# Kernel optimization log

Measured on AMD Instinct MI355X. Metric: run time of the kernel, lower is better.

The kernel has to match this reference:

```python
import jax, jax.numpy as jnp
import numpy as np

L, D, F, H, E, V = 16, 256, 512, 8, 12, 52000  # layers, width, FFWidth, heads, experts, vocab
B, S = 4, 512
HD = D // H
EPS = 1e-5


def _ln(x, s, b):
    m = x.mean(-1, keepdims=True)
    v = ((x - m) ** 2).mean(-1, keepdims=True)
    return (x - m) / jnp.sqrt(v + EPS) * s + b


def setup_inputs() -> dict:
    key = jax.random.key(0)
    ks = jax.random.split(key, 12)
    w = lambda k, shape: (jax.random.normal(k, shape, dtype=jnp.float32) * 0.02)
    return {
        "tokens": jax.random.randint(ks[0], (B, S), 0, V),
        "emb": w(ks[1], (V, D)),
        "Wq": w(ks[2], (L, D, D)), "bq": jnp.zeros((L, D), jnp.float32),
        "Wk": w(ks[3], (L, D, D)), "bk": jnp.zeros((L, D), jnp.float32),
        "Wv": w(ks[4], (L, D, D)), "bv": jnp.zeros((L, D), jnp.float32),
        "ln1_s": jnp.ones((L, D), jnp.float32), "ln1_b": jnp.zeros((L, D), jnp.float32),
        "ln2_s": jnp.ones((L, D), jnp.float32), "ln2_b": jnp.zeros((L, D), jnp.float32),
        "gW": w(ks[5], (L, D, E)), "gb": jnp.zeros((L, E), jnp.float32),
        "ff1W": w(ks[6], (L, E, D, F)), "ff1b": jnp.zeros((L, E, F), jnp.float32),
        "ffGW": w(ks[7], (L, E, D, F)), "ffGb": jnp.zeros((L, E, F), jnp.float32),
        "ff2W": w(ks[8], (L, E, F, D)), "ff2b": jnp.zeros((L, E, D), jnp.float32),
    }


def _forward(tokens, emb, Wq, bq, Wk, bk, Wv, bv, ln1_s, ln1_b, ln2_s, ln2_b,
             gW, gb, ff1W, ff1b, ffGW, ffGb, ff2W, ff2b):
    x = emb[tokens]  # [B,S,D]
    causal = jnp.triu(jnp.full((S, S), -jnp.inf, dtype=x.dtype), 1)

    def body(x, p):
        (wq, bq_, wk, bk_, wv, bv_, l1s, l1b, l2s, l2b,
         gw, gb_, f1w, f1b, fgw, fgb, f2w, f2b) = p
        q = (x @ wq + bq_).reshape(B, S, H, HD)
        k = (x @ wk + bk_).reshape(B, S, H, HD)
        v = (x @ wv + bv_).reshape(B, S, H, HD)
        # NOTE: original applies no 1/sqrt(d) scaling -- kept faithful
        att = jnp.einsum('bshw,bShw->bhsS', q, k) + causal
        att = jax.nn.softmax(att, axis=-1)
        o = jnp.einsum('bhsS,bShw->bshw', att, v).reshape(B, S, D)
        norm = _ln(o + x, l1s, l1b)
        # MoE: top-2 experts, outputs SUMMED (no gate weighting, per original)
        probs = jax.nn.softmax(norm @ gw + gb_, axis=-1)
        _, idx = jax.lax.top_k(probs, 2)  # [B,S,2]
        msk = jax.nn.one_hot(idx, E, dtype=norm.dtype).sum(-2)  # [B,S,E] in {0,1}
        h = jax.nn.silu(jnp.einsum('bsd,edf->bsef', norm, f1w) + f1b) \
            * (jnp.einsum('bsd,edf->bsef', norm, fgw) + fgb)
        y = jnp.einsum('bsef,efd->bsed', h, f2w) + f2b
        moe = jnp.einsum('bsed,bse->bsd', y, msk)
        return _ln(moe + norm, l2s, l2b), None

    x, _ = jax.lax.scan(body, x, (Wq, bq, Wk, bk, Wv, bv, ln1_s, ln1_b, ln2_s, ln2_b,
                                  gW, gb, ff1W, ff1b, ffGW, ffGb, ff2W, ff2b))
    return x


def reference(tokens, emb, Wq, bq, Wk, bk, Wv, bv, ln1_s, ln1_b, ln2_s, ln2_b,
              gW, gb, ff1W, ff1b, ffGW, ffGb, ff2W, ff2b):
    return _forward(tokens, emb, Wq, bq, Wk, bk, Wv, bv, ln1_s, ln1_b, ln2_s, ln2_b,
                    gW, gb, ff1W, ff1b, ffGW, ffGb, ff2W, ff2b)
```

## Files before the change

kernel.cpp:

```cpp
#include <hip/hip_runtime.h>
#include <math.h>

#define LNUM 16
#define D 256
#define FF 512
#define NH 8
#define NE 12
#define HD 32
#define BB 4
#define SS 512
#define NT 2048
#define EPS 1e-5f
#define CAP 512
#define ROWSP (NE * CAP)

typedef _Float16 f16;
typedef __attribute__((ext_vector_type(8))) _Float16 f16x8;
typedef __attribute__((ext_vector_type(4))) _Float16 f16x4;
typedef __attribute__((ext_vector_type(4))) float f32x4;
#define MFMA(A, B, C) __builtin_amdgcn_mfma_f32_16x16x32_f16((A), (B), (C), 0, 0, 0)

__device__ inline void splitf(float x, f16& h, f16& l) {
  f16 hh = (f16)x;
  h = hh;
  l = (f16)(x - (float)hh);
}

__global__ __launch_bounds__(256) void k_wprep(const float* __restrict__ src,
                                               f16* __restrict__ dh, f16* __restrict__ dl,
                                               int K, int N) {
  const size_t msz = (size_t)K * N * blockIdx.z;
  src += msz; dh += msz; dl += msz;
  const int n0 = blockIdx.x * 32, k0 = blockIdx.y * 32;
  __shared__ f16 th[32][36], tl[32][36];
  const int t = threadIdx.x;
  {
    const int r = t >> 3, c4 = (t & 7) * 4;
    float4 v = *(const float4*)(src + (size_t)(k0 + r) * N + n0 + c4);
    f16 h0, l0, h1, l1, h2, l2, h3, l3;
    splitf(v.x, h0, l0); splitf(v.y, h1, l1);
    splitf(v.z, h2, l2); splitf(v.w, h3, l3);
    th[c4 + 0][r] = h0; tl[c4 + 0][r] = l0;
    th[c4 + 1][r] = h1; tl[c4 + 1][r] = l1;
    th[c4 + 2][r] = h2; tl[c4 + 2][r] = l2;
    th[c4 + 3][r] = h3; tl[c4 + 3][r] = l3;
  }
  __syncthreads();
  const int rn = t >> 3, ck = (t & 7) * 4;
  f16x4 hv, lv;
#pragma unroll
  for (int j = 0; j < 4; j++) { hv[j] = th[rn][ck + j]; lv[j] = tl[rn][ck + j]; }
  *(f16x4*)(dh + (size_t)(n0 + rn) * K + k0 + ck) = hv;
  *(f16x4*)(dl + (size_t)(n0 + rn) * K + k0 + ck) = lv;
}

__global__ __launch_bounds__(256) void k_embed(const int* __restrict__ tok,
                                               const float* __restrict__ emb,
                                               float* __restrict__ x,
                                               f16* __restrict__ xh, f16* __restrict__ xl,
                                               int* __restrict__ cntbuf) {
  int n = blockIdx.x, t = threadIdx.x;
  if (n == 0 && t < LNUM * NE) cntbuf[t] = 0;
  float val = emb[(size_t)tok[n] * D + t];
  x[(size_t)n * D + t] = val;
  f16 h, l; splitf(val, h, l);
  xh[(size_t)n * D + t] = h;
  xl[(size_t)n * D + t] = l;
}

__global__ __launch_bounds__(256) void k_qkv_mfma(
    const f16* __restrict__ xh, const f16* __restrict__ xl,
    const f16* __restrict__ wqh, const f16* __restrict__ wql, const float* __restrict__ bq,
    const f16* __restrict__ wkh, const f16* __restrict__ wkl, const float* __restrict__ bk,
    const f16* __restrict__ wvh, const f16* __restrict__ wvl, const float* __restrict__ bv,
    f16* __restrict__ qhb, f16* __restrict__ qlb,
    f16* __restrict__ khb, f16* __restrict__ klb,
    f16* __restrict__ vhb, f16* __restrict__ vlb) {
  const int mat = blockIdx.z;
  const f16* Wh; const f16* Wl; const float* bias; f16* outh; f16* outl;
  if (mat == 0)      { Wh = wqh; Wl = wql; bias = bq; outh = qhb; outl = qlb; }
  else if (mat == 1) { Wh = wkh; Wl = wkl; bias = bk; outh = khb; outl = klb; }
  else               { Wh = wvh; Wl = wvl; bias = bv; outh = vhb; outl = vlb; }
  const int row0 = blockIdx.x * 128, col0 = blockIdx.y * 64;
  __shared__ f16 Ah[128][44], Al[128][44], Bh[64][44], Bl[64][44];
  const int tid = threadIdx.x;
  const int asr = tid >> 1, asc = (tid & 1) * 16;
  const int bn2 = tid >> 2, bkc = (tid & 3) * 8;
  const int lane = tid & 63, w = tid >> 6;
  const int lm = lane & 15, lg = lane >> 4, lk = lg * 8;
  f32x4 acc[2][4] = {};
  for (int k0 = 0; k0 < D; k0 += 32) {
    {
      size_t ga = (size_t)(row0 + asr) * D + k0 + asc;
      *(f16x8*)&Ah[asr][asc]     = *(const f16x8*)(xh + ga);
      *(f16x8*)&Ah[asr][asc + 8] = *(const f16x8*)(xh + ga + 8);
      *(f16x8*)&Al[asr][asc]     = *(const f16x8*)(xl + ga);
      *(f16x8*)&Al[asr][asc + 8] = *(const f16x8*)(xl + ga + 8);
      size_t gb = (size_t)(col0 + bn2) * D + k0 + bkc;
      *(f16x8*)&Bh[bn2][bkc] = *(const f16x8*)(Wh + gb);
      *(f16x8*)&Bl[bn2][bkc] = *(const f16x8*)(Wl + gb);
    }
    __syncthreads();
    f16x8 a_h[2], a_l[2];
#pragma unroll
    for (int mt = 0; mt < 2; mt++) {
      a_h[mt] = *(const f16x8*)&Ah[w * 32 + mt * 16 + lm][lk];
      a_l[mt] = *(const f16x8*)&Al[w * 32 + mt * 16 + lm][lk];
    }
#pragma unroll
    for (int nt = 0; nt < 4; nt++) {
      f16x8 b_h = *(const f16x8*)&Bh[nt * 16 + lm][lk];
      f16x8 b_l = *(const f16x8*)&Bl[nt * 16 + lm][lk];
#pragma unroll
      for (int mt = 0; mt < 2; mt++) {
        f32x4 c = acc[mt][nt];
        c = MFMA(a_h[mt], b_h, c);
        c = MFMA(a_h[mt], b_l, c);
        c = MFMA(a_l[mt], b_h, c);
        acc[mt][nt] = c;
      }
    }
    __syncthreads();
  }
#pragma unroll
  for (int mt = 0; mt < 2; mt++)
#pragma unroll
    for (int nt = 0; nt < 4; nt++) {
      int col = col0 + nt * 16 + lm;
      float bv_ = bias[col];
#pragma unroll
      for (int r = 0; r < 4; r++) {
        int row = row0 + w * 32 + mt * 16 + lg * 4 + r;
        float val = acc[mt][nt][r] + bv_;
        f16 h16, l16; splitf(val, h16, l16);
        outh[(size_t)row * D + col] = h16;
        outl[(size_t)row * D + col] = l16;
      }
    }
}

__global__ __launch_bounds__(256) void k_attn_mfma(
    const f16* __restrict__ qh, const f16* __restrict__ ql,
    const f16* __restrict__ kh, const f16* __restrict__ kl,
    const f16* __restrict__ vh, const f16* __restrict__ vl,
    float* __restrict__ o) {
  const int rt = blockIdx.x, bh = blockIdx.y;
  const int b = bh >> 3, h = bh & 7;
  const int row0 = rt * 64;
  __shared__ f16 Qh[64][40], Ql[64][40], Kh[64][40], Kl[64][40];
  __shared__ f16 Vth[32][72], Vtl[32][72];
  __shared__ f16 Ph[4][16][72], Pl[4][16][72];
  const int tid = threadIdx.x;
  const int lane = tid & 63, w = tid >> 6;
  const int lm = lane & 15, lg = lane >> 4, lk = lg * 8;
  const int sr = tid >> 2, sc = (tid & 3) * 8;
  {
    size_t gq = (size_t)(b * SS + row0 + sr) * D + h * HD + sc;
    *(f16x8*)&Qh[sr][sc] = *(const f16x8*)(qh + gq);
    *(f16x8*)&Ql[sr][sc] = *(const f16x8*)(ql + gq);
  }
  f32x4 accO[2] = {};
  float mrow[4], lsum[4];
#pragma unroll
  for (int r = 0; r < 4; r++) { mrow[r] = -1e30f; lsum[r] = 0.f; }
  for (int ct = 0; ct <= rt; ct++) {
    __syncthreads();
    {
      size_t gk = (size_t)(b * SS + ct * 64 + sr) * D + h * HD + sc;
      *(f16x8*)&Kh[sr][sc] = *(const f16x8*)(kh + gk);
      *(f16x8*)&Kl[sr][sc] = *(const f16x8*)(kl + gk);
      f16x8 hv = *(const f16x8*)(vh + gk);
      f16x8 lv = *(const f16x8*)(vl + gk);
#pragma unroll
      for (int j = 0; j < 8; j++) { Vth[sc + j][sr] = hv[j]; Vtl[sc + j][sr] = lv[j]; }
    }
    __syncthreads();
    f16x8 qfh = *(const f16x8*)&Qh[w * 16 + lm][lk];
    f16x8 qfl = *(const f16x8*)&Ql[w * 16 + lm][lk];
    f32x4 s[4];
    __builtin_amdgcn_s_setprio(1);
#pragma unroll
    for (int nt = 0; nt < 4; nt++) {
      f16x8 kfh = *(const f16x8*)&Kh[nt * 16 + lm][lk];
      f16x8 kfl = *(const f16x8*)&Kl[nt * 16 + lm][lk];
      f32x4 c = {};
      c = MFMA(qfh, kfh, c);
      c = MFMA(qfh, kfl, c);
      c = MFMA(qfl, kfh, c);
      s[nt] = c;
    }
    __builtin_amdgcn_s_setprio(0);
    if (ct == rt) {
#pragma unroll
      for (int nt = 0; nt < 4; nt++)
#pragma unroll
        for (int r = 0; r < 4; r++)
          if (nt * 16 + lm > w * 16 + lg * 4 + r) s[nt][r] = -1e30f;
    }
    float scal[4];
#pragma unroll
    for (int r = 0; r < 4; r++) {
      float mt2 = fmaxf(fmaxf(s[0][r], s[1][r]), fmaxf(s[2][r], s[3][r]));
      mt2 = fmaxf(mt2, __shfl_xor(mt2, 1));
      mt2 = fmaxf(mt2, __shfl_xor(mt2, 2));
      mt2 = fmaxf(mt2, __shfl_xor(mt2, 4));
      mt2 = fmaxf(mt2, __shfl_xor(mt2, 8));
      float mn = fmaxf(mrow[r], mt2);
      scal[r] = expf(mrow[r] - mn);
      mrow[r] = mn;
    }
    float rs[4] = {0.f, 0.f, 0.f, 0.f};
#pragma unroll
    for (int nt = 0; nt < 4; nt++)
#pragma unroll
      for (int r = 0; r < 4; r++) {
        float pv = expf(s[nt][r] - mrow[r]);
        rs[r] += pv;
        f16 ph16, pl16; splitf(pv, ph16, pl16);
        Ph[w][lg * 4 + r][nt * 16 + lm] = ph16;
        Pl[w][lg * 4 + r][nt * 16 + lm] = pl16;
      }
#pragma unroll
    for (int r = 0; r < 4; r++) {
      rs[r] += __shfl_xor(rs[r], 1);
      rs[r] += __shfl_xor(rs[r], 2);
      rs[r] += __shfl_xor(rs[r], 4);
      rs[r] += __shfl_xor(rs[r], 8);
      lsum[r] = lsum[r] * scal[r] + rs[r];
      accO[0][r] *= scal[r];
      accO[1][r] *= scal[r];
    }
    __builtin_amdgcn_s_setprio(1);
#pragma unroll
    for (int ct2 = 0; ct2 < 2; ct2++)
#pragma unroll
      for (int ks = 0; ks < 2; ks++) {
        f16x8 pa_h = *(const f16x8*)&Ph[w][lm][ks * 32 + lk];
        f16x8 pa_l = *(const f16x8*)&Pl[w][lm][ks * 32 + lk];
        f16x8 vb_h = *(const f16x8*)&Vth[ct2 * 16 + lm][ks * 32 + lk];
        f16x8 vb_l = *(const f16x8*)&Vtl[ct2 * 16 + lm][ks * 32 + lk];
        accO[ct2] = MFMA(pa_h, vb_h, accO[ct2]);
        accO[ct2] = MFMA(pa_h, vb_l, accO[ct2]);
        accO[ct2] = MFMA(pa_l, vb_h, accO[ct2]);
      }
    __builtin_amdgcn_s_setprio(0);
  }
#pragma unroll
  for (int ct2 = 0; ct2 < 2; ct2++)
#pragma unroll
    for (int r = 0; r < 4; r++) {
      int grow = row0 + w * 16 + lg * 4 + r;
      o[(size_t)(b * SS + grow) * D + h * HD + ct2 * 16 + lm] = accO[ct2][r] / lsum[r];
    }
}

__global__ __launch_bounds__(256) void k_ln1gate(
    const float* __restrict__ o, const float* __restrict__ x,
    const float* __restrict__ s1, const float* __restrict__ b1,
    const float* __restrict__ gW, const float* __restrict__ gb,
    float* __restrict__ norm, f16* __restrict__ nhb, f16* __restrict__ nlb,
    int* __restrict__ cnt, int* __restrict__ rlist, int* __restrict__ tokpos) {
  const int w = threadIdx.x >> 6, lane = threadIdx.x & 63;
  const int n = blockIdx.x * 4 + w;
  float val[4], s1v = 0.f, s2v = 0.f;
#pragma unroll
  for (int j = 0; j < 4; j++) {
    int d = lane + 64 * j;
    float v = o[(size_t)n * D + d] + x[(size_t)n * D + d];
    val[j] = v; s1v += v; s2v += v * v;
  }
#pragma unroll
  for (int m = 1; m < 64; m <<= 1) {
    s1v += __shfl_xor(s1v, m);
    s2v += __shfl_xor(s2v, m);
  }
  float mean = s1v * (1.f / D);
  float var = s2v * (1.f / D) - mean * mean;
  float rstd = rsqrtf(var + EPS);
  float ge[NE];
#pragma unroll
  for (int e = 0; e < NE; e++) ge[e] = 0.f;
#pragma unroll
  for (int j = 0; j < 4; j++) {
    int d = lane + 64 * j;
    float nv = (val[j] - mean) * rstd * s1[d] + b1[d];
    norm[(size_t)n * D + d] = nv;
    f16 h16, l16; splitf(nv, h16, l16);
    nhb[(size_t)n * D + d] = h16;
    nlb[(size_t)n * D + d] = l16;
    const float* gr = gW + (size_t)d * NE;
#pragma unroll
    for (int e = 0; e < NE; e++) ge[e] += nv * gr[e];
  }
#pragma unroll
  for (int m = 1; m < 64; m <<= 1)
#pragma unroll
    for (int e = 0; e < NE; e++) ge[e] += __shfl_xor(ge[e], m);
  if (lane == 0) {
#pragma unroll
    for (int e = 0; e < NE; e++) ge[e] += gb[e];
    int i1 = 0; float v1 = ge[0];
#pragma unroll
    for (int e = 1; e < NE; e++) if (ge[e] > v1) { v1 = ge[e]; i1 = e; }
    int i2 = -1; float v2 = -3.4e38f;
#pragma unroll
    for (int e = 0; e < NE; e++) if (e != i1 && ge[e] > v2) { v2 = ge[e]; i2 = e; }
    int p1 = atomicAdd(&cnt[i1], 1);
    int row1 = i1 * CAP + p1;
    rlist[row1] = n;
    tokpos[n * 2 + 0] = row1;
    int p2 = atomicAdd(&cnt[i2], 1);
    int row2 = i2 * CAP + p2;
    rlist[row2] = n;
    tokpos[n * 2 + 1] = row2;
  }
}

__global__ __launch_bounds__(256) void k_ff1_mfma(
    const f16* __restrict__ nhb, const f16* __restrict__ nlb,
    const int* __restrict__ cnt, const int* __restrict__ rlist,
    const f16* __restrict__ w1th, const f16* __restrict__ w1tl, const float* __restrict__ b1f,
    const f16* __restrict__ wgth, const f16* __restrict__ wgtl, const float* __restrict__ bgf,
    f16* __restrict__ hhb, f16* __restrict__ hlb) {
  const int e = blockIdx.x >> 2, tl = blockIdx.x & 3;
  const int cnt_e = cnt[e];
  if (tl * 128 >= cnt_e) return;
  const int nv0 = cnt_e - tl * 128;
  const int nv = nv0 < 128 ? nv0 : 128;
  const int base = e * CAP + tl * 128;
  const int col0 = blockIdx.y * 64;
  const f16* W1h = w1th + (size_t)e * D * FF + (size_t)col0 * D;
  const f16* W1l = w1tl + (size_t)e * D * FF + (size_t)col0 * D;
  const f16* Wgh = wgth + (size_t)e * D * FF + (size_t)col0 * D;
  const f16* Wgl = wgtl + (size_t)e * D * FF + (size_t)col0 * D;
  __shared__ f16 Ah[128][44], Al[128][44];
  __shared__ f16 B1h[64][44], B1l[64][44], B2h[64][44], B2l[64][44];
  __shared__ int rows[128];
  const int tid = threadIdx.x;
  if (tid < 128) rows[tid] = (tid < nv) ? rlist[base + tid] : 0;
  __syncthreads();
  const int asr = tid >> 1, asc = (tid & 1) * 16;
  const int bn2 = tid >> 2, bkc = (tid & 3) * 8;
  const int lane = tid & 63, w = tid >> 6;
  const int lm = lane & 15, lg = lane >> 4, lk = lg * 8;
  f32x4 acc1[2][4] = {}, acc2[2][4] = {};
  const int arow = rows[asr];
  for (int k0 = 0; k0 < D; k0 += 32) {
    {
      size_t ga = (size_t)arow * D + k0 + asc;
      *(f16x8*)&Ah[asr][asc]     = *(const f16x8*)(nhb + ga);
      *(f16x8*)&Ah[asr][asc + 8] = *(const f16x8*)(nhb + ga + 8);
      *(f16x8*)&Al[asr][asc]     = *(const f16x8*)(nlb + ga);
      *(f16x8*)&Al[asr][asc + 8] = *(const f16x8*)(nlb + ga + 8);
      size_t gb = (size_t)bn2 * D + k0 + bkc;
      *(f16x8*)&B1h[bn2][bkc] = *(const f16x8*)(W1h + gb);
      *(f16x8*)&B1l[bn2][bkc] = *(const f16x8*)(W1l + gb);
      *(f16x8*)&B2h[bn2][bkc] = *(const f16x8*)(Wgh + gb);
      *(f16x8*)&B2l[bn2][bkc] = *(const f16x8*)(Wgl + gb);
    }
    __syncthreads();
    f16x8 a_h[2], a_l[2];
#pragma unroll
    for (int mt = 0; mt < 2; mt++) {
      a_h[mt] = *(const f16x8*)&Ah[w * 32 + mt * 16 + lm][lk];
      a_l[mt] = *(const f16x8*)&Al[w * 32 + mt * 16 + lm][lk];
    }
#pragma unroll
    for (int nt = 0; nt < 4; nt++) {
      f16x8 b_h = *(const f16x8*)&B1h[nt * 16 + lm][lk];
      f16x8 b_l = *(const f16x8*)&B1l[nt * 16 + lm][lk];
      f16x8 c_h = *(const f16x8*)&B2h[nt * 16 + lm][lk];
      f16x8 c_l = *(const f16x8*)&B2l[nt * 16 + lm][lk];
#pragma unroll
      for (int mt = 0; mt < 2; mt++) {
        f32x4 c1 = acc1[mt][nt];
        c1 = MFMA(a_h[mt], b_h, c1);
        c1 = MFMA(a_h[mt], b_l, c1);
        c1 = MFMA(a_l[mt], b_h, c1);
        acc1[mt][nt] = c1;
        f32x4 c2 = acc2[mt][nt];
        c2 = MFMA(a_h[mt], c_h, c2);
        c2 = MFMA(a_h[mt], c_l, c2);
        c2 = MFMA(a_l[mt], c_h, c2);
        acc2[mt][nt] = c2;
      }
    }
    __syncthreads();
  }
#pragma unroll
  for (int mt = 0; mt < 2; mt++)
#pragma unroll
    for (int nt = 0; nt < 4; nt++) {
      int col = col0 + nt * 16 + lm;
      float bb1 = b1f[e * FF + col], bb2 = bgf[e * FF + col];
#pragma unroll
      for (int r = 0; r < 4; r++) {
        int rit = w * 32 + mt * 16 + lg * 4 + r;
        if (rit < nv) {
          float z1 = acc1[mt][nt][r] + bb1;
          float zg = acc2[mt][nt][r] + bb2;
          float sl = z1 / (1.f + expf(-z1));
          float hv = sl * zg;
          f16 h16, l16; splitf(hv, h16, l16);
          hhb[(size_t)(base + rit) * FF + col] = h16;
          hlb[(size_t)(base + rit) * FF + col] = l16;
        }
      }
    }
}

__global__ __launch_bounds__(256) void k_ff2_mfma(
    const f16* __restrict__ hhb, const f16* __restrict__ hlb,
    const int* __restrict__ cnt,
    const f16* __restrict__ w2th, const f16* __restrict__ w2tl, const float* __restrict__ b2f,
    float* __restrict__ ybuf) {
  const int e = blockIdx.x >> 2, tl = blockIdx.x & 3;
  const int cnt_e = cnt[e];
  if (tl * 128 >= cnt_e) return;
  const int nv0 = cnt_e - tl * 128;
  const int nv = nv0 < 128 ? nv0 : 128;
  const int base = e * CAP + tl * 128;
  const int col0 = blockIdx.y * 64;
  const f16* W2h = w2th + (size_t)e * FF * D + (size_t)col0 * FF;
  const f16* W2l = w2tl + (size_t)e * FF * D + (size_t)col0 * FF;
  __shared__ f16 Ah[128][44], Al[128][44], Bh[64][44], Bl[64][44];
  const int tid = threadIdx.x;
  const int asr = tid >> 1, asc = (tid & 1) * 16;
  const int bn2 = tid >> 2, bkc = (tid & 3) * 8;
  const int lane = tid & 63, w = tid >> 6;
  const int lm = lane & 15, lg = lane >> 4, lk = lg * 8;
  f32x4 acc[2][4] = {};
  for (int k0 = 0; k0 < FF; k0 += 32) {
    {
      size_t ga = (size_t)(base + asr) * FF + k0 + asc;
      *(f16x8*)&Ah[asr][asc]     = *(const f16x8*)(hhb + ga);
      *(f16x8*)&Ah[asr][asc + 8] = *(const f16x8*)(hhb + ga + 8);
      *(f16x8*)&Al[asr][asc]     = *(const f16x8*)(hlb + ga);
      *(f16x8*)&Al[asr][asc + 8] = *(const f16x8*)(hlb + ga + 8);
      size_t gb = (size_t)bn2 * FF + k0 + bkc;
      *(f16x8*)&Bh[bn2][bkc] = *(const f16x8*)(W2h + gb);
      *(f16x8*)&Bl[bn2][bkc] = *(const f16x8*)(W2l + gb);
    }
    __syncthreads();
    f16x8 a_h[2], a_l[2];
#pragma unroll
    for (int mt = 0; mt < 2; mt++) {
      a_h[mt] = *(const f16x8*)&Ah[w * 32 + mt * 16 + lm][lk];
      a_l[mt] = *(const f16x8*)&Al[w * 32 + mt * 16 + lm][lk];
    }
#pragma unroll
    for (int nt = 0; nt < 4; nt++) {
      f16x8 b_h = *(const f16x8*)&Bh[nt * 16 + lm][lk];
      f16x8 b_l = *(const f16x8*)&Bl[nt * 16 + lm][lk];
#pragma unroll
      for (int mt = 0; mt < 2; mt++) {
        f32x4 c = acc[mt][nt];
        c = MFMA(a_h[mt], b_h, c);
        c = MFMA(a_h[mt], b_l, c);
        c = MFMA(a_l[mt], b_h, c);
        acc[mt][nt] = c;
      }
    }
    __syncthreads();
  }
#pragma unroll
  for (int mt = 0; mt < 2; mt++)
#pragma unroll
    for (int nt = 0; nt < 4; nt++) {
      int col = col0 + nt * 16 + lm;
      float bb = b2f[e * D + col];
#pragma unroll
      for (int r = 0; r < 4; r++) {
        int rit = w * 32 + mt * 16 + lg * 4 + r;
        if (rit < nv) ybuf[(size_t)(base + rit) * D + col] = acc[mt][nt][r] + bb;
      }
    }
}

__global__ __launch_bounds__(256) void k_ln2(
    const float* __restrict__ ybuf, const int* __restrict__ tokpos,
    const float* __restrict__ norm, const float* __restrict__ s2, const float* __restrict__ b2,
    float* __restrict__ dst, f16* __restrict__ xh, f16* __restrict__ xl) {
  const int w = threadIdx.x >> 6, lane = threadIdx.x & 63;
  const int n = blockIdx.x * 4 + w;
  const int p0 = tokpos[n * 2 + 0], p1 = tokpos[n * 2 + 1];
  float val[4], s1v = 0.f, s2v = 0.f;
#pragma unroll
  for (int j = 0; j < 4; j++) {
    int d = lane + 64 * j;
    float v = ybuf[(size_t)p0 * D + d] + ybuf[(size_t)p1 * D + d] + norm[(size_t)n * D + d];
    val[j] = v; s1v += v; s2v += v * v;
  }
#pragma unroll
  for (int m = 1; m < 64; m <<= 1) {
    s1v += __shfl_xor(s1v, m);
    s2v += __shfl_xor(s2v, m);
  }
  float mean = s1v * (1.f / D);
  float var = s2v * (1.f / D) - mean * mean;
  float rstd = rsqrtf(var + EPS);
#pragma unroll
  for (int j = 0; j < 4; j++) {
    int d = lane + 64 * j;
    float ov = (val[j] - mean) * rstd * s2[d] + b2[d];
    dst[(size_t)n * D + d] = ov;
    f16 h16, l16; splitf(ov, h16, l16);
    xh[(size_t)n * D + d] = h16;
    xl[(size_t)n * D + d] = l16;
  }
}

extern "C" void kernel_launch(void* const* d_in, const int* in_sizes, int n_in,
                              void* d_out, int out_size, void* d_ws, size_t ws_size,
                              hipStream_t stream) {
  (void)in_sizes; (void)n_in; (void)out_size; (void)ws_size;
  const int*   tok = (const int*)d_in[0];
  const float* emb = (const float*)d_in[1];
  const float* Wq  = (const float*)d_in[2];
  const float* bq  = (const float*)d_in[3];
  const float* Wk  = (const float*)d_in[4];
  const float* bk  = (const float*)d_in[5];
  const float* Wv  = (const float*)d_in[6];
  const float* bv  = (const float*)d_in[7];
  const float* l1s = (const float*)d_in[8];
  const float* l1b = (const float*)d_in[9];
  const float* l2s = (const float*)d_in[10];
  const float* l2b = (const float*)d_in[11];
  const float* gW  = (const float*)d_in[12];
  const float* gb  = (const float*)d_in[13];
  const float* f1W = (const float*)d_in[14];
  const float* f1b = (const float*)d_in[15];
  const float* fgW = (const float*)d_in[16];
  const float* fgb = (const float*)d_in[17];
  const float* f2W = (const float*)d_in[18];
  const float* f2b = (const float*)d_in[19];
  float* out = (float*)d_out;

  char* p = (char*)d_ws;
  auto alloc = [&](size_t bytes) { char* r = p; p += (bytes + 255) & ~(size_t)255; return r; };
  float* xb = (float*)alloc((size_t)NT * D * 4);
  f16* xh = (f16*)alloc((size_t)NT * D * 2);
  f16* xl = (f16*)alloc((size_t)NT * D * 2);
  f16* qhb = (f16*)alloc((size_t)NT * D * 2);
  f16* qlb = (f16*)alloc((size_t)NT * D * 2);
  f16* khb = (f16*)alloc((size_t)NT * D * 2);
  f16* klb = (f16*)alloc((size_t)NT * D * 2);
  f16* vhb = (f16*)alloc((size_t)NT * D * 2);
  f16* vlb = (f16*)alloc((size_t)NT * D * 2);
  float* ob = (float*)alloc((size_t)NT * D * 4);
  float* nb = (float*)alloc((size_t)NT * D * 4);
  f16* nhb = (f16*)alloc((size_t)NT * D * 2);
  f16* nlb = (f16*)alloc((size_t)NT * D * 2);
  f16* hhb = (f16*)alloc((size_t)ROWSP * FF * 2);
  f16* hlb = (f16*)alloc((size_t)ROWSP * FF * 2);
  float* yb = (float*)alloc((size_t)ROWSP * D * 4);
  int* cntbuf = (int*)alloc((size_t)LNUM * NE * 4);
  int* rlist  = (int*)alloc((size_t)ROWSP * 4);
  int* tokpos = (int*)alloc((size_t)NT * 2 * 4);
  size_t qkvsz = (size_t)LNUM * D * D;
  size_t ffsz  = (size_t)LNUM * NE * D * FF;
  f16* wqh = (f16*)alloc(qkvsz * 2); f16* wql = (f16*)alloc(qkvsz * 2);
  f16* wkh = (f16*)alloc(qkvsz * 2); f16* wkl = (f16*)alloc(qkvsz * 2);
  f16* wvh = (f16*)alloc(qkvsz * 2); f16* wvl = (f16*)alloc(qkvsz * 2);
  f16* w1th = (f16*)alloc(ffsz * 2); f16* w1tl = (f16*)alloc(ffsz * 2);
  f16* wgth = (f16*)alloc(ffsz * 2); f16* wgtl = (f16*)alloc(ffsz * 2);
  f16* w2th = (f16*)alloc(ffsz * 2); f16* w2tl = (f16*)alloc(ffsz * 2);

  k_wprep<<<dim3(D / 32, D / 32, LNUM), 256, 0, stream>>>(Wq, wqh, wql, D, D);
  k_wprep<<<dim3(D / 32, D / 32, LNUM), 256, 0, stream>>>(Wk, wkh, wkl, D, D);
  k_wprep<<<dim3(D / 32, D / 32, LNUM), 256, 0, stream>>>(Wv, wvh, wvl, D, D);
  k_wprep<<<dim3(FF / 32, D / 32, LNUM * NE), 256, 0, stream>>>(f1W, w1th, w1tl, D, FF);
  k_wprep<<<dim3(FF / 32, D / 32, LNUM * NE), 256, 0, stream>>>(fgW, wgth, wgtl, D, FF);
  k_wprep<<<dim3(D / 32, FF / 32, LNUM * NE), 256, 0, stream>>>(f2W, w2th, w2tl, FF, D);

  k_embed<<<NT, 256, 0, stream>>>(tok, emb, xb, xh, xl, cntbuf);

  for (int l = 0; l < LNUM; l++) {
    int* cnt = cntbuf + l * NE;
    k_qkv_mfma<<<dim3(16, 4, 3), 256, 0, stream>>>(
        xh, xl,
        wqh + (size_t)l * D * D, wql + (size_t)l * D * D, bq + (size_t)l * D,
        wkh + (size_t)l * D * D, wkl + (size_t)l * D * D, bk + (size_t)l * D,
        wvh + (size_t)l * D * D, wvl + (size_t)l * D * D, bv + (size_t)l * D,
        qhb, qlb, khb, klb, vhb, vlb);
    k_attn_mfma<<<dim3(8, 32), 256, 0, stream>>>(qhb, qlb, khb, klb, vhb, vlb, ob);
    k_ln1gate<<<NT / 4, 256, 0, stream>>>(ob, xb, l1s + (size_t)l * D, l1b + (size_t)l * D,
                                          gW + (size_t)l * D * NE, gb + (size_t)l * NE,
                                          nb, nhb, nlb, cnt, rlist, tokpos);
    k_ff1_mfma<<<dim3(NE * 4, 8), 256, 0, stream>>>(
        nhb, nlb, cnt, rlist,
        w1th + (size_t)l * NE * D * FF, w1tl + (size_t)l * NE * D * FF, f1b + (size_t)l * NE * FF,
        wgth + (size_t)l * NE * D * FF, wgtl + (size_t)l * NE * D * FF, fgb + (size_t)l * NE * FF,
        hhb, hlb);
    k_ff2_mfma<<<dim3(NE * 4, 4), 256, 0, stream>>>(
        hhb, hlb, cnt,
        w2th + (size_t)l * NE * FF * D, w2tl + (size_t)l * NE * FF * D, f2b + (size_t)l * NE * D,
        yb);
    k_ln2<<<NT / 4, 256, 0, stream>>>(yb, tokpos, nb, l2s + (size_t)l * D, l2b + (size_t)l * D,
                                      (l == LNUM - 1) ? out : xb, xh, xl);
  }
}
```

Baseline: 2.461 ms.

## Fuse per-layer kernels into a persistent megakernel with software grid barriers

Replaces the roughly 96 per-layer kernel launches with one persistent 256-block kernel. Stages (embed, QKV, attention, LN1/gate, routing, FF1, FF2, LN2) are separated by atomic-counter grid barriers, and shared memory is a union across stages. MoE routing now uses compacted padded per-expert tiles instead of fixed per-expert capacity, so FF work scales with actual expert load. This removes launch gaps and tail idling, at the cost of relying on all 256 blocks being co-resident; the barrier also has a spin timeout that could silently break correctness.

```diff
diff --git a/kernel.cpp b/kernel.cpp
--- a/kernel.cpp
+++ b/kernel.cpp
@@ -11,8 +11,9 @@
 #define SS 512
 #define NT 2048
 #define EPS 1e-5f
-#define CAP 512
-#define ROWSP (NE * CAP)
+#define MAXT 48
+#define PADROWS 5632
+#define GRIDN 256
 
 typedef _Float16 f16;
 typedef __attribute__((ext_vector_type(8))) _Float16 f16x8;
@@ -25,6 +26,29 @@
   h = hh;
   l = (f16)(x - (float)hh);
 }
+
+__device__ inline void gridbar(int* cnt, int* gen) {
+  __syncthreads();
+  if (threadIdx.x == 0) {
+    __threadfence();
+    int g = __hip_atomic_load(gen, __ATOMIC_RELAXED, __HIP_MEMORY_SCOPE_AGENT);
+    int a = __hip_atomic_fetch_add(cnt, 1, __ATOMIC_ACQ_REL, __HIP_MEMORY_SCOPE_AGENT);
+    if (a == GRIDN - 1) {
+      __hip_atomic_store(cnt, 0, __ATOMIC_RELAXED, __HIP_MEMORY_SCOPE_AGENT);
+      __hip_atomic_fetch_add(gen, 1, __ATOMIC_ACQ_REL, __HIP_MEMORY_SCOPE_AGENT);
+    } else {
+      int spins = 0;
+      while (__hip_atomic_load(gen, __ATOMIC_ACQUIRE, __HIP_MEMORY_SCOPE_AGENT) == g) {
+        __builtin_amdgcn_s_sleep(2);
+        if (++spins > (1 << 17)) break;
+      }
+    }
+    __threadfence();
+  }
+  __syncthreads();
+}
+
+__global__ void k_bzero(int* bcnt) { *bcnt = 0; }
 
 __global__ __launch_bounds__(256) void k_wprep(const float* __restrict__ src,
                                                f16* __restrict__ dh, f16* __restrict__ dl,
@@ -32,7 +56,7 @@
   const size_t msz = (size_t)K * N * blockIdx.z;
   src += msz; dh += msz; dl += msz;
   const int n0 = blockIdx.x * 32, k0 = blockIdx.y * 32;
-  __shared__ f16 th[32][36], tl[32][36];
+  __shared__ f16 th[32][33], tl[32][33];
   const int t = threadIdx.x;
   {
     const int r = t >> 3, c4 = (t & 7) * 4;
@@ -54,459 +78,503 @@
   *(f16x4*)(dl + (size_t)(n0 + rn) * K + k0 + ck) = lv;
 }
 
-__global__ __launch_bounds__(256) void k_embed(const int* __restrict__ tok,
-                                               const float* __restrict__ emb,
-                                               float* __restrict__ x,
-                                               f16* __restrict__ xh, f16* __restrict__ xl,
-                                               int* __restrict__ cntbuf) {
-  int n = blockIdx.x, t = threadIdx.x;
-  if (n == 0 && t < LNUM * NE) cntbuf[t] = 0;
-  float val = emb[(size_t)tok[n] * D + t];
-  x[(size_t)n * D + t] = val;
-  f16 h, l; splitf(val, h, l);
-  xh[(size_t)n * D + t] = h;
-  xl[(size_t)n * D + t] = l;
-}
-
-__global__ __launch_bounds__(256) void k_qkv_mfma(
-    const f16* __restrict__ xh, const f16* __restrict__ xl,
-    const f16* __restrict__ wqh, const f16* __restrict__ wql, const float* __restrict__ bq,
-    const f16* __restrict__ wkh, const f16* __restrict__ wkl, const float* __restrict__ bk,
-    const f16* __restrict__ wvh, const f16* __restrict__ wvl, const float* __restrict__ bv,
-    f16* __restrict__ qhb, f16* __restrict__ qlb,
-    f16* __restrict__ khb, f16* __restrict__ klb,
-    f16* __restrict__ vhb, f16* __restrict__ vlb) {
-  const int mat = blockIdx.z;
-  const f16* Wh; const f16* Wl; const float* bias; f16* outh; f16* outl;
-  if (mat == 0)      { Wh = wqh; Wl = wql; bias = bq; outh = qhb; outl = qlb; }
-  else if (mat == 1) { Wh = wkh; Wl = wkl; bias = bk; outh = khb; outl = klb; }
-  else               { Wh = wvh; Wl = wvl; bias = bv; outh = vhb; outl = vlb; }
-  const int row0 = blockIdx.x * 128, col0 = blockIdx.y * 64;
-  __shared__ f16 Ah[128][44], Al[128][44], Bh[64][44], Bl[64][44];
-  const int tid = threadIdx.x;
-  const int asr = tid >> 1, asc = (tid & 1) * 16;
-  const int bn2 = tid >> 2, bkc = (tid & 3) * 8;
-  const int lane = tid & 63, w = tid >> 6;
-  const int lm = lane & 15, lg = lane >> 4, lk = lg * 8;
-  f32x4 acc[2][4] = {};
-  for (int k0 = 0; k0 < D; k0 += 32) {
-    {
-      size_t ga = (size_t)(row0 + asr) * D + k0 + asc;
-      *(f16x8*)&Ah[asr][asc]     = *(const f16x8*)(xh + ga);
-      *(f16x8*)&Ah[asr][asc + 8] = *(const f16x8*)(xh + ga + 8);
-      *(f16x8*)&Al[asr][asc]     = *(const f16x8*)(xl + ga);
-      *(f16x8*)&Al[asr][asc + 8] = *(const f16x8*)(xl + ga + 8);
-      size_t gb = (size_t)(col0 + bn2) * D + k0 + bkc;
-      *(f16x8*)&Bh[bn2][bkc] = *(const f16x8*)(Wh + gb);
-      *(f16x8*)&Bl[bn2][bkc] = *(const f16x8*)(Wl + gb);
-    }
-    __syncthreads();
-    f16x8 a_h[2], a_l[2];
-#pragma unroll
-    for (int mt = 0; mt < 2; mt++) {
-      a_h[mt] = *(const f16x8*)&Ah[w * 32 + mt * 16 + lm][lk];
-      a_l[mt] = *(const f16x8*)&Al[w * 32 + mt * 16 + lm][lk];
-    }
-#pragma unroll
-    for (int nt = 0; nt < 4; nt++) {
-      f16x8 b_h = *(const f16x8*)&Bh[nt * 16 + lm][lk];
-      f16x8 b_l = *(const f16x8*)&Bl[nt * 16 + lm][lk];
-#pragma unroll
-      for (int mt = 0; mt < 2; mt++) {
-        f32x4 c = acc[mt][nt];
-        c = MFMA(a_h[mt], b_h, c);
-        c = MFMA(a_h[mt], b_l, c);
-        c = MFMA(a_l[mt], b_h, c);
-        acc[mt][nt] = c;
-      }
-    }
-    __syncthreads();
-  }
-#pragma unroll
-  for (int mt = 0; mt < 2; mt++)
-#pragma unroll
-    for (int nt = 0; nt < 4; nt++) {
-      int col = col0 + nt * 16 + lm;
-      float bv_ = bias[col];
-#pragma unroll
-      for (int r = 0; r < 4; r++) {
-        int row = row0 + w * 32 + mt * 16 + lg * 4 + r;
-        float val = acc[mt][nt][r] + bv_;
-        f16 h16, l16; splitf(val, h16, l16);
-        outh[(size_t)row * D + col] = h16;
-        outl[(size_t)row * D + col] = l16;
-      }
-    }
-}
-
-__global__ __launch_bounds__(256) void k_attn_mfma(
-    const f16* __restrict__ qh, const f16* __restrict__ ql,
-    const f16* __restrict__ kh, const f16* __restrict__ kl,
-    const f16* __restrict__ vh, const f16* __restrict__ vl,
-    float* __restrict__ o) {
-  const int rt = blockIdx.x, bh = blockIdx.y;
-  const int b = bh >> 3, h = bh & 7;
-  const int row0 = rt * 64;
-  __shared__ f16 Qh[64][40], Ql[64][40], Kh[64][40], Kl[64][40];
-  __shared__ f16 Vth[32][72], Vtl[32][72];
-  __shared__ f16 Ph[4][16][72], Pl[4][16][72];
+struct QkvS { f16 Ah[128][44]; f16 Al[128][44]; f16 Bh[64][44]; f16 Bl[64][44]; };
+struct AttnS {
+  f16 Qh[64][40]; f16 Ql[64][40]; f16 Kh[64][40]; f16 Kl[64][40];
+  f16 Vth[32][72]; f16 Vtl[32][72];
+  f16 Ph[4][16][72]; f16 Pl[4][16][72];
+};
+struct Ff1S {
+  f16 Ah[128][44]; f16 Al[128][44];
+  f16 B1h[64][44]; f16 B1l[64][44]; f16 B2h[64][44]; f16 B2l[64][44];
+  int rows[128];
+};
+struct Ff2S { f16 Ah[128][44]; f16 Al[128][44]; f16 Bh[64][44]; f16 Bl[64][44]; };
+struct RouteS { int cnt[NE]; int cur[NE]; int poff[NE]; };
+union SmemU { QkvS q; AttnS a; Ff1S f1; Ff2S f2; RouteS r; };
+
+struct MP {
+  const int* tok; const float* emb;
+  const float *bq, *bk, *bv;
+  const float *l1s, *l1b, *l2s, *l2b, *gW, *gb;
+  const float *f1b, *fgb, *f2b;
+  const f16 *wqh, *wql, *wkh, *wkl, *wvh, *wvl;
+  const f16 *w1th, *w1tl, *wgth, *wgtl, *w2th, *w2tl;
+  float *xb, *ob, *nb, *yb, *out;
+  f16 *xh, *xl, *qhb, *qlb, *khb, *klb, *vhb, *vlb, *nhb, *nlb, *hhb, *hlb;
+  int *eidx, *rlist, *tokpos, *te, *tbase, *tnv;
+  int *bcnt, *bgen;
+};
+
+__global__ __launch_bounds__(256, 1) void k_mega(MP P) {
+  __shared__ SmemU sm;
+  const int bid = blockIdx.x;
   const int tid = threadIdx.x;
   const int lane = tid & 63, w = tid >> 6;
   const int lm = lane & 15, lg = lane >> 4, lk = lg * 8;
-  const int sr = tid >> 2, sc = (tid & 3) * 8;
-  {
-    size_t gq = (size_t)(b * SS + row0 + sr) * D + h * HD + sc;
-    *(f16x8*)&Qh[sr][sc] = *(const f16x8*)(qh + gq);
-    *(f16x8*)&Ql[sr][sc] = *(const f16x8*)(ql + gq);
+
+  for (int n = bid; n < NT; n += GRIDN) {
+    float val = P.emb[(size_t)P.tok[n] * D + tid];
+    P.xb[(size_t)n * D + tid] = val;
+    f16 h, l; splitf(val, h, l);
+    P.xh[(size_t)n * D + tid] = h;
+    P.xl[(size_t)n * D + tid] = l;
   }
-  f32x4 accO[2] = {};
-  float mrow[4], lsum[4];
-#pragma unroll
-  for (int r = 0; r < 4; r++) { mrow[r] = -1e30f; lsum[r] = 0.f; }
-  for (int ct = 0; ct <= rt; ct++) {
-    __syncthreads();
+  gridbar(P.bcnt, P.bgen);
+
+  for (int l = 0; l < LNUM; l++) {
+    const f16* wqh = P.wqh + (size_t)l * D * D;
+    const f16* wql = P.wql + (size_t)l * D * D;
+    const f16* wkh = P.wkh + (size_t)l * D * D;
+    const f16* wkl = P.wkl + (size_t)l * D * D;
+    const f16* wvh = P.wvh + (size_t)l * D * D;
+    const f16* wvl = P.wvl + (size_t)l * D * D;
+    const float* bq = P.bq + (size_t)l * D;
+    const float* bk = P.bk + (size_t)l * D;
+    const float* bv = P.bv + (size_t)l * D;
+    const float* l1s = P.l1s + (size_t)l * D;
+    const float* l1b = P.l1b + (size_t)l * D;
+    const float* l2s = P.l2s + (size_t)l * D;
+    const float* l2b = P.l2b + (size_t)l * D;
+    const float* gW = P.gW + (size_t)l * D * NE;
+    const float* gb = P.gb + (size_t)l * NE;
+    const f16* w1th = P.w1th + (size_t)l * NE * D * FF;
+    const f16* w1tl = P.w1tl + (size_t)l * NE * D * FF;
+    const f16* wgth = P.wgth + (size_t)l * NE * D * FF;
+    const f16* wgtl = P.wgtl + (size_t)l * NE * D * FF;
+    const f16* w2th = P.w2th + (size_t)l * NE * FF * D;
+    const f16* w2tl = P.w2tl + (size_t)l * NE * FF * D;
+    const float* b1f = P.f1b + (size_t)l * NE * FF;
+    const float* bgf = P.fgb + (size_t)l * NE * FF;
+    const float* b2f = P.f2b + (size_t)l * NE * D;
+
+    if (bid < 192) {
+      const int bx = bid & 15, by = (bid >> 4) & 3, mat = bid >> 6;
+      const f16* Wh; const f16* Wl; const float* bias; f16* outh; f16* outl;
+      if (mat == 0)      { Wh = wqh; Wl = wql; bias = bq; outh = P.qhb; outl = P.qlb; }
+      else if (mat == 1) { Wh = wkh; Wl = wkl; bias = bk; outh = P.khb; outl = P.klb; }
+      else               { Wh = wvh; Wl = wvl; bias = bv; outh = P.vhb; outl = P.vlb; }
+      const int row0 = bx * 128, col0 = by * 64;
+      const int asr = tid >> 1, asc = (tid & 1) * 16;
+      const int bn2 = tid >> 2, bkc = (tid & 3) * 8;
+      f32x4 acc[2][4] = {};
+      for (int k0 = 0; k0 < D; k0 += 32) {
+        {
+          size_t ga = (size_t)(row0 + asr) * D + k0 + asc;
+          *(f16x8*)&sm.q.Ah[asr][asc]     = *(const f16x8*)(P.xh + ga);
+          *(f16x8*)&sm.q.Ah[asr][asc + 8] = *(const f16x8*)(P.xh + ga + 8);
+          *(f16x8*)&sm.q.Al[asr][asc]     = *(const f16x8*)(P.xl + ga);
+          *(f16x8*)&sm.q.Al[asr][asc + 8] = *(const f16x8*)(P.xl + ga + 8);
+          size_t gb2 = (size_t)(col0 + bn2) * D + k0 + bkc;
+          *(f16x8*)&sm.q.Bh[bn2][bkc] = *(const f16x8*)(Wh + gb2);
+          *(f16x8*)&sm.q.Bl[bn2][bkc] = *(const f16x8*)(Wl + gb2);
+        }
+        __syncthreads();
+        f16x8 a_h[2], a_l[2];
+#pragma unroll
+        for (int mt = 0; mt < 2; mt++) {
+          a_h[mt] = *(const f16x8*)&sm.q.Ah[w * 32 + mt * 16 + lm][lk];
+          a_l[mt] = *(const f16x8*)&sm.q.Al[w * 32 + mt * 16 + lm][lk];
+        }
+#pragma unroll
+        for (int nt = 0; nt < 4; nt++) {
+          f16x8 b_h = *(const f16x8*)&sm.q.Bh[nt * 16 + lm][lk];
+          f16x8 b_l = *(const f16x8*)&sm.q.Bl[nt * 16 + lm][lk];
+#pragma unroll
+          for (int mt = 0; mt < 2; mt++) {
+            f32x4 c = acc[mt][nt];
+            c = MFMA(a_h[mt], b_h, c);
+            c = MFMA(a_h[mt], b_l, c);
+            c = MFMA(a_l[mt], b_h, c);
+            acc[mt][nt] = c;
+          }
+        }
+        __syncthreads();
+      }
+#pragma unroll
+      for (int mt = 0; mt < 2; mt++)
+#pragma unroll
+        for (int nt = 0; nt < 4; nt++) {
+          int col = col0 + nt * 16 + lm;
+          float bv_ = bias[col];
+#pragma unroll
+          for (int r = 0; r < 4; r++) {
+            int row = row0 + w * 32 + mt * 16 + lg * 4 + r;
+            float val = acc[mt][nt][r] + bv_;
+            f16 h16, l16; splitf(val, h16, l16);
+            outh[(size_t)row * D + col] = h16;
+            outl[(size_t)row * D + col] = l16;
+          }
+        }
+    }
+    gridbar(P.bcnt, P.bgen);
+
     {
-      size_t gk = (size_t)(b * SS + ct * 64 + sr) * D + h * HD + sc;
-      *(f16x8*)&Kh[sr][sc] = *(const f16x8*)(kh + gk);
-      *(f16x8*)&Kl[sr][sc] = *(const f16x8*)(kl + gk);
-      f16x8 hv = *(const f16x8*)(vh + gk);
-      f16x8 lv = *(const f16x8*)(vl + gk);
-#pragma unroll
-      for (int j = 0; j < 8; j++) { Vth[sc + j][sr] = hv[j]; Vtl[sc + j][sr] = lv[j]; }
-    }
-    __syncthreads();
-    f16x8 qfh = *(const f16x8*)&Qh[w * 16 + lm][lk];
-    f16x8 qfl = *(const f16x8*)&Ql[w * 16 + lm][lk];
-    f32x4 s[4];
-    __builtin_amdgcn_s_setprio(1);
-#pragma unroll
-    for (int nt = 0; nt < 4; nt++) {
-      f16x8 kfh = *(const f16x8*)&Kh[nt * 16 + lm][lk];
-      f16x8 kfl = *(const f16x8*)&Kl[nt * 16 + lm][lk];
-      f32x4 c = {};
-      c = MFMA(qfh, kfh, c);
-      c = MFMA(qfh, kfl, c);
-      c = MFMA(qfl, kfh, c);
-      s[nt] = c;
-    }
-    __builtin_amdgcn_s_setprio(0);
-    if (ct == rt) {
-#pragma unroll
-      for (int nt = 0; nt < 4; nt++)
-#pragma unroll
-        for (int r = 0; r < 4; r++)
-          if (nt * 16 + lm > w * 16 + lg * 4 + r) s[nt][r] = -1e30f;
-    }
-    float scal[4];
-#pragma unroll
-    for (int r = 0; r < 4; r++) {
-      float mt2 = fmaxf(fmaxf(s[0][r], s[1][r]), fmaxf(s[2][r], s[3][r]));
-      mt2 = fmaxf(mt2, __shfl_xor(mt2, 1));
-      mt2 = fmaxf(mt2, __shfl_xor(mt2, 2));
-      mt2 = fmaxf(mt2, __shfl_xor(mt2, 4));
-      mt2 = fmaxf(mt2, __shfl_xor(mt2, 8));
-      float mn = fmaxf(mrow[r], mt2);
-      scal[r] = expf(mrow[r] - mn);
-      mrow[r] = mn;
-    }
-    float rs[4] = {0.f, 0.f, 0.f, 0.f};
-#pragma unroll
-    for (int nt = 0; nt < 4; nt++)
-#pragma unroll
-      for (int r = 0; r < 4; r++) {
-        float pv = expf(s[nt][r] - mrow[r]);
-        rs[r] += pv;
-        f16 ph16, pl16; splitf(pv, ph16, pl16);
-        Ph[w][lg * 4 + r][nt * 16 + lm] = ph16;
-        Pl[w][lg * 4 + r][nt * 16 + lm] = pl16;
-      }
-#pragma unroll
-    for (int r = 0; r < 4; r++) {
-      rs[r] += __shfl_xor(rs[r], 1);
-      rs[r] += __shfl_xor(rs[r], 2);
-      rs[r] += __shfl_xor(rs[r], 4);
-      rs[r] += __shfl_xor(rs[r], 8);
-      lsum[r] = lsum[r] * scal[r] + rs[r];
-      accO[0][r] *= scal[r];
-      accO[1][r] *= scal[r];
-    }
-    __builtin_amdgcn_s_setprio(1);
-#pragma unroll
-    for (int ct2 = 0; ct2 < 2; ct2++)
-#pragma unroll
-      for (int ks = 0; ks < 2; ks++) {
-        f16x8 pa_h = *(const f16x8*)&Ph[w][lm][ks * 32 + lk];
-        f16x8 pa_l = *(const f16x8*)&Pl[w][lm][ks * 32 + lk];
-        f16x8 vb_h = *(const f16x8*)&Vth[ct2 * 16 + lm][ks * 32 + lk];
-        f16x8 vb_l = *(const f16x8*)&Vtl[ct2 * 16 + lm][ks * 32 + lk];
-        accO[ct2] = MFMA(pa_h, vb_h, accO[ct2]);
-        accO[ct2] = MFMA(pa_h, vb_l, accO[ct2]);
-        accO[ct2] = MFMA(pa_l, vb_h, accO[ct2]);
-      }
-    __builtin_amdgcn_s_setprio(0);
-  }
-#pragma unroll
-  for (int ct2 = 0; ct2 < 2; ct2++)
-#pragma unroll
-    for (int r = 0; r < 4; r++) {
-      int grow = row0 + w * 16 + lg * 4 + r;
-      o[(size_t)(b * SS + grow) * D + h * HD + ct2 * 16 + lm] = accO[ct2][r] / lsum[r];
-    }
-}
-
-__global__ __launch_bounds__(256) void k_ln1gate(
-    const float* __restrict__ o, const float* __restrict__ x,
-    const float* __restrict__ s1, const float* __restrict__ b1,
-    const float* __restrict__ gW, const float* __restrict__ gb,
-    float* __restrict__ norm, f16* __restrict__ nhb, f16* __restrict__ nlb,
-    int* __restrict__ cnt, int* __restrict__ rlist, int* __restrict__ tokpos) {
-  const int w = threadIdx.x >> 6, lane = threadIdx.x & 63;
-  const int n = blockIdx.x * 4 + w;
-  float val[4], s1v = 0.f, s2v = 0.f;
-#pragma unroll
-  for (int j = 0; j < 4; j++) {
-    int d = lane + 64 * j;
-    float v = o[(size_t)n * D + d] + x[(size_t)n * D + d];
-    val[j] = v; s1v += v; s2v += v * v;
-  }
-#pragma unroll
-  for (int m = 1; m < 64; m <<= 1) {
-    s1v += __shfl_xor(s1v, m);
-    s2v += __shfl_xor(s2v, m);
-  }
-  float mean = s1v * (1.f / D);
-  float var = s2v * (1.f / D) - mean * mean;
-  float rstd = rsqrtf(var + EPS);
-  float ge[NE];
-#pragma unroll
-  for (int e = 0; e < NE; e++) ge[e] = 0.f;
-#pragma unroll
-  for (int j = 0; j < 4; j++) {
-    int d = lane + 64 * j;
-    float nv = (val[j] - mean) * rstd * s1[d] + b1[d];
-    norm[(size_t)n * D + d] = nv;
-    f16 h16, l16; splitf(nv, h16, l16);
-    nhb[(size_t)n * D + d] = h16;
-    nlb[(size_t)n * D + d] = l16;
-    const float* gr = gW + (size_t)d * NE;
-#pragma unroll
-    for (int e = 0; e < NE; e++) ge[e] += nv * gr[e];
-  }
-#pragma unroll
-  for (int m = 1; m < 64; m <<= 1)
-#pragma unroll
-    for (int e = 0; e < NE; e++) ge[e] += __shfl_xor(ge[e], m);
-  if (lane == 0) {
-#pragma unroll
-    for (int e = 0; e < NE; e++) ge[e] += gb[e];
-    int i1 = 0; float v1 = ge[0];
-#pragma unroll
-    for (int e = 1; e < NE; e++) if (ge[e] > v1) { v1 = ge[e]; i1 = e; }
-    int i2 = -1; float v2 = -3.4e38f;
-#pragma unroll
-    for (int e = 0; e < NE; e++) if (e != i1 && ge[e] > v2) { v2 = ge[e]; i2 = e; }
-    int p1 = atomicAdd(&cnt[i1], 1);
-    int row1 = i1 * CAP + p1;
-    rlist[row1] = n;
-    tokpos[n * 2 + 0] = row1;
-    int p2 = atomicAdd(&cnt[i2], 1);
-    int row2 = i2 * CAP + p2;
-    rlist[row2] = n;
-    tokpos[n * 2 + 1] = row2;
-  }
-}
-
-__global__ __launch_bounds__(256) void k_ff1_mfma(
-    const f16* __restrict__ nhb, const f16* __restrict__ nlb,
-    const int* __restrict__ cnt, const int* __restrict__ rlist,
-    const f16* __restrict__ w1th, const f16* __restrict__ w1tl, const float* __restrict__ b1f,
-    const f16* __restrict__ wgth, const f16* __restrict__ wgtl, const float* __restrict__ bgf,
-    f16* __restrict__ hhb, f16* __restrict__ hlb) {
-  const int e = blockIdx.x >> 2, tl = blockIdx.x & 3;
-  const int cnt_e = cnt[e];
-  if (tl * 128 >= cnt_e) return;
-  const int nv0 = cnt_e - tl * 128;
-  const int nv = nv0 < 128 ? nv0 : 128;
-  const int base = e * CAP + tl * 128;
-  const int col0 = blockIdx.y * 64;
-  const f16* W1h = w1th + (size_t)e * D * FF + (size_t)col0 * D;
-  const f16* W1l = w1tl + (size_t)e * D * FF + (size_t)col0 * D;
-  const f16* Wgh = wgth + (size_t)e * D * FF + (size_t)col0 * D;
-  const f16* Wgl = wgtl + (size_t)e * D * FF + (size_t)col0 * D;
-  __shared__ f16 Ah[128][44], Al[128][44];
-  __shared__ f16 B1h[64][44], B1l[64][44], B2h[64][44], B2l[64][44];
-  __shared__ int rows[128];
-  const int tid = threadIdx.x;
-  if (tid < 128) rows[tid] = (tid < nv) ? rlist[base + tid] : 0;
-  __syncthreads();
-  const int asr = tid >> 1, asc = (tid & 1) * 16;
-  const int bn2 = tid >> 2, bkc = (tid & 3) * 8;
-  const int lane = tid & 63, w = tid >> 6;
-  const int lm = lane & 15, lg = lane >> 4, lk = lg * 8;
-  f32x4 acc1[2][4] = {}, acc2[2][4] = {};
-  const int arow = rows[asr];
-  for (int k0 = 0; k0 < D; k0 += 32) {
+      const int rt = bid >> 5, bh = bid & 31;
+      const int b = bh >> 3, h = bh & 7;
+      const int row0 = rt * 64;
+      const int sr = tid >> 2, sc = (tid & 3) * 8;
+      {
+        size_t gq = (size_t)(b * SS + row0 + sr) * D + h * HD + sc;
+        *(f16x8*)&sm.a.Qh[sr][sc] = *(const f16x8*)(P.qhb + gq);
+        *(f16x8*)&sm.a.Ql[sr][sc] = *(const f16x8*)(P.qlb + gq);
+      }
+      f32x4 accO[2] = {};
+      float mrow[4], lsum[4];
+#pragma unroll
+      for (int r = 0; r < 4; r++) { mrow[r] = -1e30f; lsum[r] = 0.f; }
+      for (int ct = 0; ct <= rt; ct++) {
+        __syncthreads();
+        {
+          size_t gk = (size_t)(b * SS + ct * 64 + sr) * D + h * HD + sc;
+          *(f16x8*)&sm.a.Kh[sr][sc] = *(const f16x8*)(P.khb + gk);
+          *(f16x8*)&sm.a.Kl[sr][sc] = *(const f16x8*)(P.klb + gk);
+          f16x8 hv = *(const f16x8*)(P.vhb + gk);
+          f16x8 lv = *(const f16x8*)(P.vlb + gk);
+#pragma unroll
+          for (int j = 0; j < 8; j++) { sm.a.Vth[sc + j][sr] = hv[j]; sm.a.Vtl[sc + j][sr] = lv[j]; }
+        }
+        __syncthreads();
+        f16x8 qfh = *(const f16x8*)&sm.a.Qh[w * 16 + lm][lk];
+        f16x8 qfl = *(const f16x8*)&sm.a.Ql[w * 16 + lm][lk];
+        f32x4 s[4];
+#pragma unroll
+        for (int nt = 0; nt < 4; nt++) {
+          f16x8 kfh = *(const f16x8*)&sm.a.Kh[nt * 16 + lm][lk];
+          f16x8 kfl = *(const f16x8*)&sm.a.Kl[nt * 16 + lm][lk];
+          f32x4 c = {};
+          c = MFMA(qfh, kfh, c);
+          c = MFMA(qfh, kfl, c);
+          c = MFMA(qfl, kfh, c);
+          s[nt] = c;
+        }
+        if (ct == rt) {
+#pragma unroll
+          for (int nt = 0; nt < 4; nt++)
+#pragma unroll
+            for (int r = 0; r < 4; r++)
+              if (nt * 16 + lm > w * 16 + lg * 4 + r) s[nt][r] = -1e30f;
+        }
+        float scal[4];
+#pragma unroll
+        for (int r = 0; r < 4; r++) {
+          float mt2 = fmaxf(fmaxf(s[0][r], s[1][r]), fmaxf(s[2][r], s[3][r]));
+          mt2 = fmaxf(mt2, __shfl_xor(mt2, 1));
+          mt2 = fmaxf(mt2, __shfl_xor(mt2, 2));
+          mt2 = fmaxf(mt2, __shfl_xor(mt2, 4));
+          mt2 = fmaxf(mt2, __shfl_xor(mt2, 8));
+          float mn = fmaxf(mrow[r], mt2);
+          scal[r] = expf(mrow[r] - mn);
+          mrow[r] = mn;
+        }
+        float rs[4] = {0.f, 0.f, 0.f, 0.f};
+#pragma unroll
+        for (int nt = 0; nt < 4; nt++)
+#pragma unroll
+          for (int r = 0; r < 4; r++) {
+            float pv = expf(s[nt][r] - mrow[r]);
+            rs[r] += pv;
+            f16 ph16, pl16; splitf(pv, ph16, pl16);
+            sm.a.Ph[w][lg * 4 + r][nt * 16 + lm] = ph16;
+            sm.a.Pl[w][lg * 4 + r][nt * 16 + lm] = pl16;
+          }
+#pragma unroll
+        for (int r = 0; r < 4; r++) {
+          rs[r] += __shfl_xor(rs[r], 1);
+          rs[r] += __shfl_xor(rs[r], 2);
+          rs[r] += __shfl_xor(rs[r], 4);
+          rs[r] += __shfl_xor(rs[r], 8);
+          lsum[r] = lsum[r] * scal[r] + rs[r];
+          accO[0][r] *= scal[r];
+          accO[1][r] *= scal[r];
+        }
+#pragma unroll
+        for (int ct2 = 0; ct2 < 2; ct2++)
+#pragma unroll
+          for (int ks = 0; ks < 2; ks++) {
+            f16x8 pa_h = *(const f16x8*)&sm.a.Ph[w][lm][ks * 32 + lk];
+            f16x8 pa_l = *(const f16x8*)&sm.a.Pl[w][lm][ks * 32 + lk];
+            f16x8 vb_h = *(const f16x8*)&sm.a.Vth[ct2 * 16 + lm][ks * 32 + lk];
+            f16x8 vb_l = *(const f16x8*)&sm.a.Vtl[ct2 * 16 + lm][ks * 32 + lk];
+            accO[ct2] = MFMA(pa_h, vb_h, accO[ct2]);
+            accO[ct2] = MFMA(pa_h, vb_l, accO[ct2]);
+            accO[ct2] = MFMA(pa_l, vb_h, accO[ct2]);
+          }
+      }
+#pragma unroll
+      for (int ct2 = 0; ct2 < 2; ct2++)
+#pragma unroll
+        for (int r = 0; r < 4; r++) {
+          int grow = row0 + w * 16 + lg * 4 + r;
+          P.ob[(size_t)(b * SS + grow) * D + h * HD + ct2 * 16 + lm] = accO[ct2][r] / lsum[r];
+        }
+    }
+    gridbar(P.bcnt, P.bgen);
+
+    for (int g2 = 0; g2 < 2; g2++) {
+      const int n = (bid + g2 * GRIDN) * 4 + w;
+      float val[4], s1v = 0.f, s2v = 0.f;
+#pragma unroll
+      for (int j = 0; j < 4; j++) {
+        int d = lane + 64 * j;
+        float v = P.ob[(size_t)n * D + d] + P.xb[(size_t)n * D + d];
+        val[j] = v; s1v += v; s2v += v * v;
+      }
+#pragma unroll
+      for (int m = 1; m < 64; m <<= 1) {
+        s1v += __shfl_xor(s1v, m);
+        s2v += __shfl_xor(s2v, m);
+      }
+      float mean = s1v * (1.f / D);
+      float var = s2v * (1.f / D) - mean * mean;
+      float rstd = rsqrtf(var + EPS);
+      float ge[NE];
+#pragma unroll
+      for (int e = 0; e < NE; e++) ge[e] = 0.f;
+#pragma unroll
+      for (int j = 0; j < 4; j++) {
+        int d = lane + 64 * j;
+        float nv = (val[j] - mean) * rstd * l1s[d] + l1b[d];
+        P.nb[(size_t)n * D + d] = nv;
+        f16 h16, l16; splitf(nv, h16, l16);
+        P.nhb[(size_t)n * D + d] = h16;
+        P.nlb[(size_t)n * D + d] = l16;
+        const float* gr = gW + (size_t)d * NE;
+#pragma unroll
+        for (int e = 0; e < NE; e++) ge[e] += nv * gr[e];
+      }
+#pragma unroll
+      for (int m = 1; m < 64; m <<= 1)
+#pragma unroll
+        for (int e = 0; e < NE; e++) ge[e] += __shfl_xor(ge[e], m);
+      if (lane == 0) {
+#pragma unroll
+        for (int e = 0; e < NE; e++) ge[e] += gb[e];
+        int i1 = 0; float v1 = ge[0];
+#pragma unroll
+        for (int e = 1; e < NE; e++) if (ge[e] > v1) { v1 = ge[e]; i1 = e; }
+        int i2 = -1; float v2 = -3.4e38f;
+#pragma unroll
+        for (int e = 0; e < NE; e++) if (e != i1 && ge[e] > v2) { v2 = ge[e]; i2 = e; }
+        P.eidx[n * 2 + 0] = i1;
+        P.eidx[n * 2 + 1] = i2;
+      }
+    }
+    gridbar(P.bcnt, P.bgen);
+
+    if (bid == 0) {
+      if (tid < NE) { sm.r.cnt[tid] = 0; sm.r.cur[tid] = 0; }
+      __syncthreads();
+      for (int n = tid; n < NT; n += 256) {
+        atomicAdd(&sm.r.cnt[P.eidx[n * 2 + 0]], 1);
+        atomicAdd(&sm.r.cnt[P.eidx[n * 2 + 1]], 1);
+      }
+      __syncthreads();
+      if (tid == 0) {
+        int off = 0, ti = 0;
+        for (int e = 0; e < NE; e++) {
+          sm.r.poff[e] = off;
+          int ntl = (sm.r.cnt[e] + 127) >> 7;
+          for (int tt = 0; tt < ntl; tt++) {
+            P.te[ti] = e; P.tbase[ti] = off + tt * 128;
+            int rem = sm.r.cnt[e] - tt * 128; P.tnv[ti] = rem < 128 ? rem : 128;
+            ti++;
+          }
+          off += ntl * 128;
+        }
+        for (; ti < MAXT; ti++) P.te[ti] = -1;
+      }
+      __syncthreads();
+      for (int n = tid; n < NT; n += 256) {
+#pragma unroll
+        for (int s2 = 0; s2 < 2; s2++) {
+          int e = P.eidx[n * 2 + s2];
+          int pos = atomicAdd(&sm.r.cur[e], 1);
+          int row = sm.r.poff[e] + pos;
+          P.rlist[row] = n;
+          P.tokpos[n * 2 + s2] = row;
+        }
+      }
+    }
+    gridbar(P.bcnt, P.bgen);
+
+    for (int pass = 0; pass < 2; pass++) {
+      const int t = bid + pass * GRIDN;
+      bool active = (t < 384);
+      int mt0 = 0, cc = 0, e = -1;
+      if (active) { mt0 = t % 48; cc = t / 48; e = P.te[mt0]; active = (e >= 0); }
+      if (active) {
+        const int base = P.tbase[mt0], nv = P.tnv[mt0];
+        const int col0 = cc * 64;
+        const f16* W1h = w1th + (size_t)e * D * FF + (size_t)col0 * D;
+        const f16* W1l = w1tl + (size_t)e * D * FF + (size_t)col0 * D;
+        const f16* Wgh = wgth + (size_t)e * D * FF + (size_t)col0 * D;
+        const f16* Wgl = wgtl + (size_t)e * D * FF + (size_t)col0 * D;
+        if (tid < 128) sm.f1.rows[tid] = (tid < nv) ? P.rlist[base + tid] : 0;
+        __syncthreads();
+        const int asr = tid >> 1, asc = (tid & 1) * 16;
+        const int bn2 = tid >> 2, bkc = (tid & 3) * 8;
+        f32x4 acc1[2][4] = {}, acc2[2][4] = {};
+        const int arow = sm.f1.rows[asr];
+        for (int k0 = 0; k0 < D; k0 += 32) {
+          {
+            size_t ga = (size_t)arow * D + k0 + asc;
+            *(f16x8*)&sm.f1.Ah[asr][asc]     = *(const f16x8*)(P.nhb + ga);
+            *(f16x8*)&sm.f1.Ah[asr][asc + 8] = *(const f16x8*)(P.nhb + ga + 8);
+            *(f16x8*)&sm.f1.Al[asr][asc]     = *(const f16x8*)(P.nlb + ga);
+            *(f16x8*)&sm.f1.Al[asr][asc + 8] = *(const f16x8*)(P.nlb + ga + 8);
+            size_t gb2 = (size_t)bn2 * D + k0 + bkc;
+            *(f16x8*)&sm.f1.B1h[bn2][bkc] = *(const f16x8*)(W1h + gb2);
+            *(f16x8*)&sm.f1.B1l[bn2][bkc] = *(const f16x8*)(W1l + gb2);
+            *(f16x8*)&sm.f1.B2h[bn2][bkc] = *(const f16x8*)(Wgh + gb2);
+            *(f16x8*)&sm.f1.B2l[bn2][bkc] = *(const f16x8*)(Wgl + gb2);
+          }
+          __syncthreads();
+          f16x8 a_h[2], a_l[2];
+#pragma unroll
+          for (int mt = 0; mt < 2; mt++) {
+            a_h[mt] = *(const f16x8*)&sm.f1.Ah[w * 32 + mt * 16 + lm][lk];
+            a_l[mt] = *(const f16x8*)&sm.f1.Al[w * 32 + mt * 16 + lm][lk];
+          }
+#pragma unroll
+          for (int nt = 0; nt < 4; nt++) {
+            f16x8 b_h = *(const f16x8*)&sm.f1.B1h[nt * 16 + lm][lk];
+            f16x8 b_l = *(const f16x8*)&sm.f1.B1l[nt * 16 + lm][lk];
+            f16x8 c_h = *(const f16x8*)&sm.f1.B2h[nt * 16 + lm][lk];
+            f16x8 c_l = *(const f16x8*)&sm.f1.B2l[nt * 16 + lm][lk];
+#pragma unroll
+            for (int mt = 0; mt < 2; mt++) {
+              f32x4 c1 = acc1[mt][nt];
+              c1 = MFMA(a_h[mt], b_h, c1);
+              c1 = MFMA(a_h[mt], b_l, c1);
+              c1 = MFMA(a_l[mt], b_h, c1);
+              acc1[mt][nt] = c1;
+              f32x4 c2 = acc2[mt][nt];
+              c2 = MFMA(a_h[mt], c_h, c2);
+              c2 = MFMA(a_h[mt], c_l, c2);
+              c2 = MFMA(a_l[mt], c_h, c2);
+              acc2[mt][nt] = c2;
+            }
+          }
+          __syncthreads();
+        }
+#pragma unroll
+        for (int mt = 0; mt < 2; mt++)
+#pragma unroll
+          for (int nt = 0; nt < 4; nt++) {
+            int col = col0 + nt * 16 + lm;
+            float bb1 = b1f[e * FF + col], bb2 = bgf[e * FF + col];
+#pragma unroll
+            for (int r = 0; r < 4; r++) {
+              int rit = w * 32 + mt * 16 + lg * 4 + r;
+              if (rit < nv) {
+                float z1 = acc1[mt][nt][r] + bb1;
+                float zg = acc2[mt][nt][r] + bb2;
+                float sl = z1 / (1.f + expf(-z1));
+                float hv = sl * zg;
+                f16 h16, l16; splitf(hv, h16, l16);
+                P.hhb[(size_t)(base + rit) * FF + col] = h16;
+                P.hlb[(size_t)(base + rit) * FF + col] = l16;
+              }
+            }
+          }
+      }
+    }
+    gridbar(P.bcnt, P.bgen);
+
     {
-      size_t ga = (size_t)arow * D + k0 + asc;
-      *(f16x8*)&Ah[asr][asc]     = *(const f16x8*)(nhb + ga);
-      *(f16x8*)&Ah[asr][asc + 8] = *(const f16x8*)(nhb + ga + 8);
-      *(f16x8*)&Al[asr][asc]     = *(const f16x8*)(nlb + ga);
-      *(f16x8*)&Al[asr][asc + 8] = *(const f16x8*)(nlb + ga + 8);
-      size_t gb = (size_t)bn2 * D + k0 + bkc;
-      *(f16x8*)&B1h[bn2][bkc] = *(const f16x8*)(W1h + gb);
-      *(f16x8*)&B1l[bn2][bkc] = *(const f16x8*)(W1l + gb);
-      *(f16x8*)&B2h[bn2][bkc] = *(const f16x8*)(Wgh + gb);
-      *(f16x8*)&B2l[bn2][bkc] = *(const f16x8*)(Wgl + gb);
-    }
-    __syncthreads();
-    f16x8 a_h[2], a_l[2];
-#pragma unroll
-    for (int mt = 0; mt < 2; mt++) {
-      a_h[mt] = *(const f16x8*)&Ah[w * 32 + mt * 16 + lm][lk];
-      a_l[mt] = *(const f16x8*)&Al[w * 32 + mt * 16 + lm][lk];
-    }
-#pragma unroll
-    for (int nt = 0; nt < 4; nt++) {
-      f16x8 b_h = *(const f16x8*)&B1h[nt * 16 + lm][lk];
-      f16x8 b_l = *(const f16x8*)&B1l[nt * 16 + lm][lk];
-      f16x8 c_h = *(const f16x8*)&B2h[nt * 16 + lm][lk];
-      f16x8 c_l = *(const f16x8*)&B2l[nt * 16 + lm][lk];
-#pragma unroll
-      for (int mt = 0; mt < 2; mt++) {
-        f32x4 c1 = acc1[mt][nt];
-        c1 = MFMA(a_h[mt], b_h, c1);
-        c1 = MFMA(a_h[mt], b_l, c1);
-        c1 = MFMA(a_l[mt], b_h, c1);
-        acc1[mt][nt] = c1;
-        f32x4 c2 = acc2[mt][nt];
-        c2 = MFMA(a_h[mt], c_h, c2);
-        c2 = MFMA(a_h[mt], c_l, c2);
-        c2 = MFMA(a_l[mt], c_h, c2);
-        acc2[mt][nt] = c2;
-      }
-    }
-    __syncthreads();
-  }
-#pragma unroll
-  for (int mt = 0; mt < 2; mt++)
-#pragma unroll
-    for (int nt = 0; nt < 4; nt++) {
-      int col = col0 + nt * 16 + lm;
-      float bb1 = b1f[e * FF + col], bb2 = bgf[e * FF + col];
-#pragma unroll
-      for (int r = 0; r < 4; r++) {
-        int rit = w * 32 + mt * 16 + lg * 4 + r;
-        if (rit < nv) {
-          float z1 = acc1[mt][nt][r] + bb1;
-          float zg = acc2[mt][nt][r] + bb2;
-          float sl = z1 / (1.f + expf(-z1));
-          float hv = sl * zg;
-          f16 h16, l16; splitf(hv, h16, l16);
-          hhb[(size_t)(base + rit) * FF + col] = h16;
-          hlb[(size_t)(base + rit) * FF + col] = l16;
-        }
-      }
-    }
-}
-
-__global__ __launch_bounds__(256) void k_ff2_mfma(
-    const f16* __restrict__ hhb, const f16* __restrict__ hlb,
-    const int* __restrict__ cnt,
-    const f16* __restrict__ w2th, const f16* __restrict__ w2tl, const float* __restrict__ b2f,
-    float* __restrict__ ybuf) {
-  const int e = blockIdx.x >> 2, tl = blockIdx.x & 3;
-  const int cnt_e = cnt[e];
-  if (tl * 128 >= cnt_e) return;
-  const int nv0 = cnt_e - tl * 128;
-  const int nv = nv0 < 128 ? nv0 : 128;
-  const int base = e * CAP + tl * 128;
-  const int col0 = blockIdx.y * 64;
-  const f16* W2h = w2th + (size_t)e * FF * D + (size_t)col0 * FF;
-  const f16* W2l = w2tl + (size_t)e * FF * D + (size_t)col0 * FF;
-  __shared__ f16 Ah[128][44], Al[128][44], Bh[64][44], Bl[64][44];
-  const int tid = threadIdx.x;
-  const int asr = tid >> 1, asc = (tid & 1) * 16;
-  const int bn2 = tid >> 2, bkc = (tid & 3) * 8;
-  const int lane = tid & 63, w = tid >> 6;
-  const int lm = lane & 15, lg = lane >> 4, lk = lg * 8;
-  f32x4 acc[2][4] = {};
-  for (int k0 = 0; k0 < FF; k0 += 32) {
+      bool active = (bid < 192);
+      int mt0 = 0, cc = 0, e = -1;
+      if (active) { mt0 = bid % 48; cc = bid / 48; e = P.te[mt0]; active = (e >= 0); }
+      if (active) {
+        const int base = P.tbase[mt0], nv = P.tnv[mt0];
+        const int col0 = cc * 64;
+        const f16* W2h = w2th + (size_t)e * FF * D + (size_t)col0 * FF;
+        const f16* W2l = w2tl + (size_t)e * FF * D + (size_t)col0 * FF;
+        const int asr = tid >> 1, asc = (tid & 1) * 16;
+        const int bn2 = tid >> 2, bkc = (tid & 3) * 8;
+        f32x4 acc[2][4] = {};
+        for (int k0 = 0; k0 < FF; k0 += 32) {
+          {
+            size_t ga = (size_t)(base + asr) * FF + k0 + asc;
+            *(f16x8*)&sm.f2.Ah[asr][asc]     = *(const f16x8*)(P.hhb + ga);
+            *(f16x8*)&sm.f2.Ah[asr][asc + 8] = *(const f16x8*)(P.hhb + ga + 8);
+            *(f16x8*)&sm.f2.Al[asr][asc]     = *(const f16x8*)(P.hlb + ga);
+            *(f16x8*)&sm.f2.Al[asr][asc + 8] = *(const f16x8*)(P.hlb + ga + 8);
+            size_t gb2 = (size_t)bn2 * FF + k0 + bkc;
+            *(f16x8*)&sm.f2.Bh[bn2][bkc] = *(const f16x8*)(W2h + gb2);
+            *(f16x8*)&sm.f2.Bl[bn2][bkc] = *(const f16x8*)(W2l + gb2);
+          }
+          __syncthreads();
+          f16x8 a_h[2], a_l[2];
+#pragma unroll
+          for (int mt = 0; mt < 2; mt++) {
+            a_h[mt] = *(const f16x8*)&sm.f2.Ah[w * 32 + mt * 16 + lm][lk];
+            a_l[mt] = *(const f16x8*)&sm.f2.Al[w * 32 + mt * 16 + lm][lk];
+          }
+#pragma unroll
+          for (int nt = 0; nt < 4; nt++) {
+            f16x8 b_h = *(const f16x8*)&sm.f2.Bh[nt * 16 + lm][lk];
+            f16x8 b_l = *(const f16x8*)&sm.f2.Bl[nt * 16 + lm][lk];
+#pragma unroll
+            for (int mt = 0; mt < 2; mt++) {
+              f32x4 c = acc[mt][nt];
+              c = MFMA(a_h[mt], b_h, c);
+              c = MFMA(a_h[mt], b_l, c);
+              c = MFMA(a_l[mt], b_h, c);
+              acc[mt][nt] = c;
+            }
+          }
+          __syncthreads();
+        }
+#pragma unroll
+        for (int mt = 0; mt < 2; mt++)
+#pragma unroll
+          for (int nt = 0; nt < 4; nt++) {
+            int col = col0 + nt * 16 + lm;
+            float bb = b2f[e * D + col];
+#pragma unroll
+            for (int r = 0; r < 4; r++) {
+              int rit = w * 32 + mt * 16 + lg * 4 + r;
+              if (rit < nv) P.yb[(size_t)(base + rit) * D + col] = acc[mt][nt][r] + bb;
+            }
+          }
+      }
+    }
+    gridbar(P.bcnt, P.bgen);
+
     {
-      size_t ga = (size_t)(base + asr) * FF + k0 + asc;
-      *(f16x8*)&Ah[asr][asc]     = *(const f16x8*)(hhb + ga);
-      *(f16x8*)&Ah[asr][asc + 8] = *(const f16x8*)(hhb + ga + 8);
-      *(f16x8*)&Al[asr][asc]     = *(const f16x8*)(hlb + ga);
-      *(f16x8*)&Al[asr][asc + 8] = *(const f16x8*)(hlb + ga + 8);
-      size_t gb = (size_t)bn2 * FF + k0 + bkc;
-      *(f16x8*)&Bh[bn2][bkc] = *(const f16x8*)(W2h + gb);
-      *(f16x8*)&Bl[bn2][bkc] = *(const f16x8*)(W2l + gb);
-    }
-    __syncthreads();
-    f16x8 a_h[2], a_l[2];
-#pragma unroll
-    for (int mt = 0; mt < 2; mt++) {
-      a_h[mt] = *(const f16x8*)&Ah[w * 32 + mt * 16 + lm][lk];
-      a_l[mt] = *(const f16x8*)&Al[w * 32 + mt * 16 + lm][lk];
-    }
-#pragma unroll
-    for (int nt = 0; nt < 4; nt++) {
-      f16x8 b_h = *(const f16x8*)&Bh[nt * 16 + lm][lk];
-      f16x8 b_l = *(const f16x8*)&Bl[nt * 16 + lm][lk];
-#pragma unroll
-      for (int mt = 0; mt < 2; mt++) {
-        f32x4 c = acc[mt][nt];
-        c = MFMA(a_h[mt], b_h, c);
-        c = MFMA(a_h[mt], b_l, c);
-        c = MFMA(a_l[mt], b_h, c);
-        acc[mt][nt] = c;
-      }
-    }
-    __syncthreads();
-  }
-#pragma unroll
-  for (int mt = 0; mt < 2; mt++)
-#pragma unroll
-    for (int nt = 0; nt < 4; nt++) {
-      int col = col0 + nt * 16 + lm;
-      float bb = b2f[e * D + col];
-#pragma unroll
-      for (int r = 0; r < 4; r++) {
-        int rit = w * 32 + mt * 16 + lg * 4 + r;
-        if (rit < nv) ybuf[(size_t)(base + rit) * D + col] = acc[mt][nt][r] + bb;
-      }
-    }
-}
-
-__global__ __launch_bounds__(256) void k_ln2(
-    const float* __restrict__ ybuf, const int* __restrict__ tokpos,
-    const float* __restrict__ norm, const float* __restrict__ s2, const float* __restrict__ b2,
-    float* __restrict__ dst, f16* __restrict__ xh, f16* __restrict__ xl) {
-  const int w = threadIdx.x >> 6, lane = threadIdx.x & 63;
-  const int n = blockIdx.x * 4 + w;
-  const int p0 = tokpos[n * 2 + 0], p1 = tokpos[n * 2 + 1];
-  float val[4], s1v = 0.f, s2v = 0.f;
-#pragma unroll
-  for (int j = 0; j < 4; j++) {
-    int d = lane + 64 * j;
-    float v = ybuf[(size_t)p0 * D + d] + ybuf[(size_t)p1 * D + d] + norm[(size_t)n * D + d];
-    val[j] = v; s1v += v; s2v += v * v;
-  }
-#pragma unroll
-  for (int m = 1; m < 64; m <<= 1) {
-    s1v += __shfl_xor(s1v, m);
-    s2v += __shfl_xor(s2v, m);
-  }
-  float mean = s1v * (1.f / D);
-  float var = s2v * (1.f / D) - mean * mean;
-  float rstd = rsqrtf(var + EPS);
-#pragma unroll
-  for (int j = 0; j < 4; j++) {
-    int d = lane + 64 * j;
-    float ov = (val[j] - mean) * rstd * s2[d] + b2[d];
-    dst[(size_t)n * D + d] = ov;
-    f16 h16, l16; splitf(ov, h16, l16);
-    xh[(size_t)n * D + d] = h16;
-    xl[(size_t)n * D + d] = l16;
+      float* dst = (l == LNUM - 1) ? P.out : P.xb;
+      for (int g2 = 0; g2 < 2; g2++) {
+        const int n = (bid + g2 * GRIDN) * 4 + w;
+        const int p0 = P.tokpos[n * 2 + 0], p1 = P.tokpos[n * 2 + 1];
+        float val[4], s1v = 0.f, s2v = 0.f;
+#pragma unroll
+        for (int j = 0; j < 4; j++) {
+          int d = lane + 64 * j;
+          float v = P.yb[(size_t)p0 * D + d] + P.yb[(size_t)p1 * D + d] + P.nb[(size_t)n * D + d];
+          val[j] = v; s1v += v; s2v += v * v;
+        }
+#pragma unroll
+        for (int m = 1; m < 64; m <<= 1) {
+          s1v += __shfl_xor(s1v, m);
+          s2v += __shfl_xor(s2v, m);
+        }
+        float mean = s1v * (1.f / D);
+        float var = s2v * (1.f / D) - mean * mean;
+        float rstd = rsqrtf(var + EPS);
+#pragma unroll
+        for (int j = 0; j < 4; j++) {
+          int d = lane + 64 * j;
+          float ov = (val[j] - mean) * rstd * l2s[d] + l2b[d];
+          dst[(size_t)n * D + d] = ov;
+          f16 h16, l16; splitf(ov, h16, l16);
+          P.xh[(size_t)n * D + d] = h16;
+          P.xl[(size_t)n * D + d] = l16;
+        }
+      }
+    }
+    gridbar(P.bcnt, P.bgen);
   }
 }
 
@@ -534,29 +602,39 @@
   const float* fgb = (const float*)d_in[17];
   const float* f2W = (const float*)d_in[18];
   const float* f2b = (const float*)d_in[19];
-  float* out = (float*)d_out;
 
   char* p = (char*)d_ws;
   auto alloc = [&](size_t bytes) { char* r = p; p += (bytes + 255) & ~(size_t)255; return r; };
-  float* xb = (float*)alloc((size_t)NT * D * 4);
-  f16* xh = (f16*)alloc((size_t)NT * D * 2);
-  f16* xl = (f16*)alloc((size_t)NT * D * 2);
-  f16* qhb = (f16*)alloc((size_t)NT * D * 2);
-  f16* qlb = (f16*)alloc((size_t)NT * D * 2);
-  f16* khb = (f16*)alloc((size_t)NT * D * 2);
-  f16* klb = (f16*)alloc((size_t)NT * D * 2);
-  f16* vhb = (f16*)alloc((size_t)NT * D * 2);
-  f16* vlb = (f16*)alloc((size_t)NT * D * 2);
-  float* ob = (float*)alloc((size_t)NT * D * 4);
-  float* nb = (float*)alloc((size_t)NT * D * 4);
-  f16* nhb = (f16*)alloc((size_t)NT * D * 2);
-  f16* nlb = (f16*)alloc((size_t)NT * D * 2);
-  f16* hhb = (f16*)alloc((size_t)ROWSP * FF * 2);
-  f16* hlb = (f16*)alloc((size_t)ROWSP * FF * 2);
-  float* yb = (float*)alloc((size_t)ROWSP * D * 4);
-  int* cntbuf = (int*)alloc((size_t)LNUM * NE * 4);
-  int* rlist  = (int*)alloc((size_t)ROWSP * 4);
-  int* tokpos = (int*)alloc((size_t)NT * 2 * 4);
+  MP P;
+  P.tok = tok; P.emb = emb;
+  P.bq = bq; P.bk = bk; P.bv = bv;
+  P.l1s = l1s; P.l1b = l1b; P.l2s = l2s; P.l2b = l2b; P.gW = gW; P.gb = gb;
+  P.f1b = f1b; P.fgb = fgb; P.f2b = f2b;
+  P.out = (float*)d_out;
+  P.xb = (float*)alloc((size_t)NT * D * 4);
+  P.xh = (f16*)alloc((size_t)NT * D * 2);
+  P.xl = (f16*)alloc((size_t)NT * D * 2);
+  P.qhb = (f16*)alloc((size_t)NT * D * 2);
+  P.qlb = (f16*)alloc((size_t)NT * D * 2);
+  P.khb = (f16*)alloc((size_t)NT * D * 2);
+  P.klb = (f16*)alloc((size_t)NT * D * 2);
+  P.vhb = (f16*)alloc((size_t)NT * D * 2);
+  P.vlb = (f16*)alloc((size_t)NT * D * 2);
+  P.ob = (float*)alloc((size_t)NT * D * 4);
+  P.nb = (float*)alloc((size_t)NT * D * 4);
+  P.nhb = (f16*)alloc((size_t)NT * D * 2);
+  P.nlb = (f16*)alloc((size_t)NT * D * 2);
+  P.hhb = (f16*)alloc((size_t)PADROWS * FF * 2);
+  P.hlb = (f16*)alloc((size_t)PADROWS * FF * 2);
+  P.yb = (float*)alloc((size_t)PADROWS * D * 4);
+  P.eidx   = (int*)alloc((size_t)NT * 2 * 4);
+  P.rlist  = (int*)alloc((size_t)PADROWS * 4);
+  P.tokpos = (int*)alloc((size_t)NT * 2 * 4);
+  P.te     = (int*)alloc(MAXT * 4);
+  P.tbase  = (int*)alloc(MAXT * 4);
+  P.tnv    = (int*)alloc(MAXT * 4);
+  P.bcnt   = (int*)alloc(256);
+  P.bgen   = (int*)alloc(256);
   size_t qkvsz = (size_t)LNUM * D * D;
   size_t ffsz  = (size_t)LNUM * NE * D * FF;
   f16* wqh = (f16*)alloc(qkvsz * 2); f16* wql = (f16*)alloc(qkvsz * 2);
@@ -565,6 +643,10 @@
   f16* w1th = (f16*)alloc(ffsz * 2); f16* w1tl = (f16*)alloc(ffsz * 2);
   f16* wgth = (f16*)alloc(ffsz * 2); f16* wgtl = (f16*)alloc(ffsz * 2);
   f16* w2th = (f16*)alloc(ffsz * 2); f16* w2tl = (f16*)alloc(ffsz * 2);
+  P.wqh = wqh; P.wql = wql; P.wkh = wkh; P.wkl = wkl; P.wvh = wvh; P.wvl = wvl;
+  P.w1th = w1th; P.w1tl = w1tl; P.wgth = wgth; P.wgtl = wgtl; P.w2th = w2th; P.w2tl = w2tl;
+
+  k_bzero<<<1, 1, 0, stream>>>(P.bcnt);
 
   k_wprep<<<dim3(D / 32, D / 32, LNUM), 256, 0, stream>>>(Wq, wqh, wql, D, D);
   k_wprep<<<dim3(D / 32, D / 32, LNUM), 256, 0, stream>>>(Wk, wkh, wkl, D, D);
@@ -573,30 +655,5 @@
   k_wprep<<<dim3(FF / 32, D / 32, LNUM * NE), 256, 0, stream>>>(fgW, wgth, wgtl, D, FF);
   k_wprep<<<dim3(D / 32, FF / 32, LNUM * NE), 256, 0, stream>>>(f2W, w2th, w2tl, FF, D);
 
-  k_embed<<<NT, 256, 0, stream>>>(tok, emb, xb, xh, xl, cntbuf);
-
-  for (int l = 0; l < LNUM; l++) {
-    int* cnt = cntbuf + l * NE;
-    k_qkv_mfma<<<dim3(16, 4, 3), 256, 0, stream>>>(
-        xh, xl,
-        wqh + (size_t)l * D * D, wql + (size_t)l * D * D, bq + (size_t)l * D,
-        wkh + (size_t)l * D * D, wkl + (size_t)l * D * D, bk + (size_t)l * D,
-        wvh + (size_t)l * D * D, wvl + (size_t)l * D * D, bv + (size_t)l * D,
-        qhb, qlb, khb, klb, vhb, vlb);
-    k_attn_mfma<<<dim3(8, 32), 256, 0, stream>>>(qhb, qlb, khb, klb, vhb, vlb, ob);
-    k_ln1gate<<<NT / 4, 256, 0, stream>>>(ob, xb, l1s + (size_t)l * D, l1b + (size_t)l * D,
-                                          gW + (size_t)l * D * NE, gb + (size_t)l * NE,
-                                          nb, nhb, nlb, cnt, rlist, tokpos);
-    k_ff1_mfma<<<dim3(NE * 4, 8), 256, 0, stream>>>(
-        nhb, nlb, cnt, rlist,
-        w1th + (size_t)l * NE * D * FF, w1tl + (size_t)l * NE * D * FF, f1b + (size_t)l * NE * FF,
-        wgth + (size_t)l * NE * D * FF, wgtl + (size_t)l * NE * D * FF, fgb + (size_t)l * NE * FF,
-        hhb, hlb);
-    k_ff2_mfma<<<dim3(NE * 4, 4), 256, 0, stream>>>(
-        hhb, hlb, cnt,
-        w2th + (size_t)l * NE * FF * D, w2tl + (size_t)l * NE * FF * D, f2b + (size_t)l * NE * D,
-        yb);
-    k_ln2<<<NT / 4, 256, 0, stream>>>(yb, tokpos, nb, l2s + (size_t)l * D, l2b + (size_t)l * D,
-                                      (l == LNUM - 1) ? out : xb, xh, xl);
-  }
+  k_mega<<<dim3(GRIDN), dim3(256), 0, stream>>>(P);
 }
```

After: 8.877 ms. 261% more time.
